# Optimization experiments

Measured on AMD Instinct MI355X. Metric: run time of the kernel, lower is better.

## Reference

```python
import jax, jax.numpy as jnp
import numpy as np

H, F = 4, 32          # num_of_heads, num_out_features
HF = H * F            # 128
F_IN = 128
EDGE_DIM = 64
HIDDEN = 256
B = 64
MLE = 1500
N = B * MLE           # 96000
E = 600000
LN_EPS = 1e-5


def setup_inputs() -> dict:
    key = jax.random.key(0)
    ks = jax.random.split(key, 20)

    def glorot(k, shape):
        fan_in, fan_out = shape[-2], shape[-1]
        lim = np.sqrt(6.0 / (fan_in + fan_out))
        return jax.random.uniform(k, shape, jnp.float32, -lim, lim)

    inp = {
        "in_nodes_features": jax.random.normal(ks[0], (N, F_IN), jnp.float32),
        "edge_index": jax.random.randint(ks[1], (2, E), 0, N),
        "edges": jax.random.normal(ks[2], (E, EDGE_DIM), jnp.float32),
        "instructions": jax.random.normal(ks[3], (B, HIDDEN), jnp.float32),
        "batch_ids": jax.random.randint(ks[4], (E,), 0, B),
        "max_local_entity": MLE,
        # parameters (stored as [in, out]; torch Linear is x @ W.T)
        "W_proj": glorot(ks[5], (F_IN, HF)),
        "W_edge": glorot(ks[6], (EDGE_DIM, HF)),
        "W_src_ins": glorot(ks[7], (HIDDEN, HF)),
        "b_src_ins": jnp.zeros((HF,), jnp.float32),
        "W_trg_ins": glorot(ks[8], (HIDDEN, HF)),
        "b_trg_ins": jnp.zeros((HF,), jnp.float32),
        "W_edge_ins": glorot(ks[9], (HIDDEN, HF)),
        "b_edge_ins": jnp.zeros((HF,), jnp.float32),
        "a_src": glorot(ks[10], (1, H, F)),
        "a_trg": glorot(ks[11], (1, H, F)),
        "a_edge": glorot(ks[12], (1, H, F)),
        "bias": jnp.zeros((HF,), jnp.float32),
        "W_skip": glorot(ks[13], (F_IN, HF)),
        "ln_gamma": jnp.ones((2 * HF,), jnp.float32),
        "ln_beta": jnp.zeros((2 * HF,), jnp.float32),
    }
    return inp


def _segment_softmax(scores, seg_idx, num_nodes):
    # scores: [E, H]; softmax over edges sharing the same seg_idx node
    s = scores - jax.lax.stop_gradient(scores.max())  # global-max shift, as in original
    e = jnp.exp(s)
    denom = jax.ops.segment_sum(e, seg_idx, num_segments=num_nodes)  # [N, H]
    return (e / (denom[seg_idx] + 1e-16))[..., None]  # [E, H, 1]


def _branch(proj, lift_idx, agg_idx, scores_per_edge, x, W_skip, bias, num_nodes):
    att = _segment_softmax(scores_per_edge, agg_idx, num_nodes)          # [E,H,1]
    weighted = proj[lift_idx] * att                                      # [E,H,F]
    out = jax.ops.segment_sum(weighted, agg_idx, num_segments=num_nodes) # [N,H,F]
    out = out + (x @ W_skip).reshape(num_nodes, H, F)                    # skip (F != F_in path)
    out = out.reshape(num_nodes, HF) + bias                              # concat heads + bias
    return out


def reference(in_nodes_features, edge_index, edges, instructions, batch_ids,
              max_local_entity, W_proj, W_edge, W_src_ins, b_src_ins,
              W_trg_ins, b_trg_ins, W_edge_ins, b_edge_ins,
              a_src, a_trg, a_edge, bias, W_skip, ln_gamma, ln_beta):
    x = in_nodes_features                      # dropout disabled (eval / p=0)
    num_nodes = x.shape[0]
    b = instructions.shape[0]
    src_idx, trg_idx = edge_index[0], edge_index[1]

    proj = (x @ W_proj).reshape(num_nodes, H, F)           # [N,H,F]
    eproj = (edges @ W_edge).reshape(-1, H, F)             # [E,H,F]

    def bridge(Wi, bi):  # instruction -> per-node [N,H,F]
        br = instructions @ Wi + bi                        # [B,HF]
        br = jnp.broadcast_to(br[:, None, :], (b, max_local_entity, HF))
        return br.reshape(num_nodes, H, F)

    src_br = bridge(W_src_ins, b_src_ins)
    trg_br = bridge(W_trg_ins, b_trg_ins)
    edge_br = (instructions @ W_edge_ins + b_edge_ins)[batch_ids].reshape(-1, H, F)

    scores_source = (proj * a_src * src_br).sum(-1)        # [N,H]
    scores_target = (proj * a_trg * trg_br).sum(-1)        # [N,H]
    scores_edge = (eproj * a_edge * edge_br).sum(-1)       # [E,H]

    scores_per_edge = jax.nn.leaky_relu(
        scores_source[src_idx] + scores_target[trg_idx] + scores_edge,
        negative_slope=0.2)                                # [E,H]

    # direction == 'all': aggregate src->trg and trg->src
    trg_feats = _branch(proj, src_idx, trg_idx, scores_per_edge, x, W_skip, bias, num_nodes)
    src_feats = _branch(proj, trg_idx, src_idx, scores_per_edge, x, W_skip, bias, num_nodes)

    out = jnp.concatenate([src_feats, trg_feats], axis=1)  # [N, 2*HF]
    mu = out.mean(-1, keepdims=True)
    var = ((out - mu) ** 2).mean(-1, keepdims=True)
    return (out - mu) * jax.lax.rsqrt(var + LN_EPS) * ln_gamma + ln_beta
```

## Files before the change

kernel.cpp:

```cpp
#include <hip/hip_runtime.h>
#include <stdint.h>

typedef unsigned short ushortT;
typedef __attribute__((ext_vector_type(8))) short short8;
typedef __attribute__((ext_vector_type(4))) float float4_;

#define HH 4
#define FF 32
#define HFD 128
#define F_IN 128
#define EDGE_DIM 64
#define HIDDEN 256
#define BB 64
#define MLE 1500
#define NN 96000
#define EEc 600000
#define CAP 32

__device__ __forceinline__ float bf_lo(uint32_t u){ return __uint_as_float(u << 16); }
__device__ __forceinline__ float bf_hi(uint32_t u){ return __uint_as_float(u & 0xffff0000u); }
__device__ __forceinline__ uint32_t f2bf(float f){
    uint32_t u = __float_as_uint(f);
    return (u + 0x7fffu + ((u >> 16) & 1u)) >> 16;
}
__device__ __forceinline__ short8 cvt8(const float* p){
    float4_ x0 = *(const float4_*)p;
    float4_ x1 = *(const float4_*)(p + 4);
    short8 r;
    r[0]=(short)f2bf(x0[0]); r[1]=(short)f2bf(x0[1]); r[2]=(short)f2bf(x0[2]); r[3]=(short)f2bf(x0[3]);
    r[4]=(short)f2bf(x1[0]); r[5]=(short)f2bf(x1[1]); r[6]=(short)f2bf(x1[2]); r[7]=(short)f2bf(x1[3]);
    return r;
}

__global__ void k_bridge(const float* ins, const float* Wsrc, const float* bsrc,
                         const float* Wtrg, const float* btrg,
                         const float* Wedg, const float* bedg,
                         const float* a_src, const float* a_trg, const float* a_edge,
                         const float* W_edge,
                         float* csrc, float* ctrg, float* Mout)
{
    __shared__ float ins_s[HIDDEN];
    __shared__ float ce_s[HFD];
    int b = blockIdx.x, t = threadIdx.x;
    const float* ip = ins + b * HIDDEN;
    ins_s[t]       = ip[t];
    ins_s[t + 128] = ip[t + 128];
    __syncthreads();
    float as = 0.f, at = 0.f, ae = 0.f;
    #pragma unroll 8
    for (int k = 0; k < HIDDEN; k++){
        float iv = ins_s[k];
        as += iv * Wsrc[k*HFD + t];
        at += iv * Wtrg[k*HFD + t];
        ae += iv * Wedg[k*HFD + t];
    }
    csrc[b*HFD + t] = (as + bsrc[t]) * a_src[t];
    ctrg[b*HFD + t] = (at + btrg[t]) * a_trg[t];
    ce_s[t] = (ae + bedg[t]) * a_edge[t];
    __syncthreads();
    #pragma unroll
    for (int rep = 0; rep < 2; rep++){
        int idx = t + rep * 128;
        int d = idx >> 2, h = idx & 3;
        float acc = 0.f;
        #pragma unroll
        for (int f = 0; f < FF; f++)
            acc += W_edge[d*HFD + h*FF + f] * ce_s[h*FF + f];
        Mout[b*256 + h*64 + d] = acc;
    }
}

__global__ void k_transpose(const float* Wp, const float* Wsk, ushortT* WcatT)
{
    int idx = blockIdx.x * 256 + threadIdx.x;
    int c = idx >> 7;
    int d = idx & 127;
    float v = (c < 128) ? Wp[d*128 + c] : Wsk[d*128 + (c - 128)];
    WcatT[c*128 + d] = (ushortT)f2bf(v);
}

__global__ __launch_bounds__(256) void k_gemm(const float* x, const ushortT* WcatT,
                                              const float* csrc, const float* ctrg,
                                              ushortT* proj, ushortT* skip,
                                              float* s_src, float* s_trg)
{
    int t = threadIdx.x;
    int w = t >> 6, lane = t & 63;
    int q = lane >> 4, n16 = lane & 15;
    size_t node = (size_t)blockIdx.x * 64 + w * 16 + n16;

    float4_ acc[16];
    #pragma unroll
    for (int j = 0; j < 16; j++) acc[j] = (float4_){0.f, 0.f, 0.f, 0.f};

    #pragma unroll
    for (int kk = 0; kk < 4; kk++){
        short8 bfrag = cvt8(x + node * 128 + kk*32 + q*8);
        #pragma unroll
        for (int j = 0; j < 16; j++){
            short8 afrag = *(const short8*)(WcatT + (size_t)(j*16 + n16) * 128 + kk*32 + q*8);
            acc[j] = __builtin_amdgcn_mfma_f32_16x16x32_bf16(afrag, bfrag, acc[j], 0, 0, 0);
        }
    }

    #pragma unroll
    for (int j = 0; j < 16; j++){
        uint32_t p0 = f2bf(acc[j][0]) | (f2bf(acc[j][1]) << 16);
        uint32_t p1 = f2bf(acc[j][2]) | (f2bf(acc[j][3]) << 16);
        ushortT* base = (j < 8) ? (proj + node*128 + j*16 + q*4)
                                : (skip + node*128 + (j-8)*16 + q*4);
        uint2 pv; pv.x = p0; pv.y = p1;
        *(uint2*)base = pv;
    }

    int b = (int)(node / MLE);
    const float* cs = csrc + b * HFD;
    const float* ct = ctrg + b * HFD;
    float ps[4] = {0,0,0,0}, pt[4] = {0,0,0,0};
    #pragma unroll
    for (int j = 0; j < 8; j++){
        int h = j >> 1;
        #pragma unroll
        for (int r = 0; r < 4; r++){
            int c = j*16 + q*4 + r;
            ps[h] += acc[j][r] * cs[c];
            pt[h] += acc[j][r] * ct[c];
        }
    }
    #pragma unroll
    for (int m = 16; m < 64; m <<= 1){
        #pragma unroll
        for (int hh = 0; hh < 4; hh++){
            ps[hh] += __shfl_xor(ps[hh], m, 64);
            pt[hh] += __shfl_xor(pt[hh], m, 64);
        }
    }
    float vs = (q == 0) ? ps[0] : (q == 1) ? ps[1] : (q == 2) ? ps[2] : ps[3];
    float vt = (q == 0) ? pt[0] : (q == 1) ? pt[1] : (q == 2) ? pt[2] : pt[3];
    s_src[node*4 + q] = vs;
    s_trg[node*4 + q] = vt;
}

__global__ __launch_bounds__(256) void k_score(const int* eidx, const int* bids,
    const float* edges, const float* M, const float* s_src, const float* s_trg,
    uint4* recs, int* head_src, int* head_trg, int* next_src, int* next_trg)
{
    int t = threadIdx.x;
    int wave = t >> 6, l = t & 63;
    int g = l >> 4, s = l & 15;
    int eb = (blockIdx.x * 4 + wave) * 16;

    int i_sel = s >> 2;
    int h_sel = s & 3;
    int e   = eb + i_sel*4 + g;
    int src = eidx[e];
    int trg = eidx[EEc + e];
    float ssv = s_src[(size_t)src*4 + h_sel];
    float stv = s_trg[(size_t)trg*4 + h_sel];

    float4_ ev[4];
    int bidv[4];
    #pragma unroll
    for (int i = 0; i < 4; i++){
        int r = i*4 + g;
        ev[i]   = *(const float4_*)(edges + (size_t)(eb + r) * 64 + s*4);
        bidv[i] = bids[eb + r];
    }

    float p00=0.f,p01=0.f,p02=0.f,p03=0.f;
    float p10=0.f,p11=0.f,p12=0.f,p13=0.f;
    float p20=0.f,p21=0.f,p22=0.f,p23=0.f;
    float p30=0.f,p31=0.f,p32=0.f,p33=0.f;
    #pragma unroll
    for (int i = 0; i < 4; i++){
        const float* Mb = M + (size_t)bidv[i] * 256;
        float4_ m0 = *(const float4_*)(Mb +   0 + s*4);
        float4_ m1 = *(const float4_*)(Mb +  64 + s*4);
        float4_ m2 = *(const float4_*)(Mb + 128 + s*4);
        float4_ m3 = *(const float4_*)(Mb + 192 + s*4);
        float4_ e4 = ev[i];
        float d0 = e4[0]*m0[0] + e4[1]*m0[1] + e4[2]*m0[2] + e4[3]*m0[3];
        float d1 = e4[0]*m1[0] + e4[1]*m1[1] + e4[2]*m1[2] + e4[3]*m1[3];
        float d2 = e4[0]*m2[0] + e4[1]*m2[1] + e4[2]*m2[2] + e4[3]*m2[3];
        float d3 = e4[0]*m3[0] + e4[1]*m3[1] + e4[2]*m3[2] + e4[3]*m3[3];
        if (i == 0){ p00=d0; p01=d1; p02=d2; p03=d3; }
        if (i == 1){ p10=d0; p11=d1; p12=d2; p13=d3; }
        if (i == 2){ p20=d0; p21=d1; p22=d2; p23=d3; }
        if (i == 3){ p30=d0; p31=d1; p32=d2; p33=d3; }
    }

    #pragma unroll
    for (int mm = 1; mm < 16; mm <<= 1){
        p00 += __shfl_xor(p00, mm, 64); p01 += __shfl_xor(p01, mm, 64);
        p02 += __shfl_xor(p02, mm, 64); p03 += __shfl_xor(p03, mm, 64);
        p10 += __shfl_xor(p10, mm, 64); p11 += __shfl_xor(p11, mm, 64);
        p12 += __shfl_xor(p12, mm, 64); p13 += __shfl_xor(p13, mm, 64);
        p20 += __shfl_xor(p20, mm, 64); p21 += __shfl_xor(p21, mm, 64);
        p22 += __shfl_xor(p22, mm, 64); p23 += __shfl_xor(p23, mm, 64);
        p30 += __shfl_xor(p30, mm, 64); p31 += __shfl_xor(p31, mm, 64);
        p32 += __shfl_xor(p32, mm, 64); p33 += __shfl_xor(p33, mm, 64);
    }

    float q0 = h_sel==0 ? p00 : h_sel==1 ? p01 : h_sel==2 ? p02 : p03;
    float q1 = h_sel==0 ? p10 : h_sel==1 ? p11 : h_sel==2 ? p12 : p13;
    float q2 = h_sel==0 ? p20 : h_sel==1 ? p21 : h_sel==2 ? p22 : p23;
    float q3 = h_sel==0 ? p30 : h_sel==1 ? p31 : h_sel==2 ? p32 : p33;
    float se = i_sel==0 ? q0 : i_sel==1 ? q1 : i_sel==2 ? q2 : q3;

    float sc = ssv + stv + se;
    sc = sc > 0.f ? sc : 0.2f * sc;
    float exv = __expf(sc);

    uint32_t my   = f2bf(exv) << ((h_sel & 1) * 16);
    uint32_t pair = my | __shfl_xor(my, 1, 64);
    uint32_t both = __shfl_xor(pair, 2, 64);

    if (h_sel == 0){
        uint4 rec;
        rec.x = (uint32_t)src; rec.y = (uint32_t)trg;
        rec.z = pair; rec.w = both;
        recs[e] = rec;
        int old0 = atomicExch(&head_src[src], e);
        next_src[e] = old0;
        int old1 = atomicExch(&head_trg[trg], e);
        next_trg[e] = old1;
    }
}

__global__ __launch_bounds__(256) void k_walk(const int* head_src, const int* head_trg,
    const int* next_src, const int* next_trg, const uint4* recs,
    int* cnt_src, int* cnt_trg, uint32_t* nbrT, uint2* evT)
{
    int id = blockIdx.x * 256 + threadIdx.x;
    int dir = (id >= NN) ? 1 : 0;
    int n = id - dir * NN;
    int e = dir ? head_trg[n] : head_src[n];
    const int* nx = dir ? next_trg : next_src;
    uint32_t* nT = nbrT + (size_t)dir * CAP * NN;
    uint2*    eT = evT  + (size_t)dir * CAP * NN;
    int c = 0;
    while (e >= 0 && c < CAP){
        uint4 r = recs[e];
        int en = nx[e];
        nT[(size_t)c*NN + n] = dir ? r.x : r.y;
        eT[(size_t)c*NN + n] = make_uint2(r.z, r.w);
        e = en;
        c++;
    }
    if (dir) cnt_trg[n] = c; else cnt_src[n] = c;
}

__global__ __launch_bounds__(256) void k_agg(const ushortT* proj, const ushortT* skip,
    const float* bias,
    const int* cnt_src, const int* cnt_trg,
    const uint32_t* nbrT, const uint2* evT,
    const float* gamma, const float* beta, float* out)
{
    __shared__ int   sh_nbr[2][4][CAP];
    __shared__ float sh_ev [2][4][CAP*4];

    int wave = threadIdx.x >> 6, lane = threadIdx.x & 63;
    int n = blockIdx.x * 4 + wave;
    int h = lane >> 4;

    int cnt0 = cnt_src[n]; if (cnt0 > CAP) cnt0 = CAP;
    int cnt1 = cnt_trg[n]; if (cnt1 > CAP) cnt1 = CAP;

    if (lane < cnt0){
        uint32_t nbr = nbrT[(size_t)lane*NN + n];
        uint2 e2     = evT [(size_t)lane*NN + n];
        sh_nbr[0][wave][lane] = (int)nbr;
        float4_ evv = { bf_lo(e2.x), bf_hi(e2.x), bf_lo(e2.y), bf_hi(e2.y) };
        *(float4_*)&sh_ev[0][wave][lane*4] = evv;
    }
    if (lane < cnt1){
        uint32_t nbr = nbrT[(size_t)(CAP + lane)*NN + n];
        uint2 e2     = evT [(size_t)(CAP + lane)*NN + n];
        sh_nbr[1][wave][lane] = (int)nbr;
        float4_ evv = { bf_lo(e2.x), bf_hi(e2.x), bf_lo(e2.y), bf_hi(e2.y) };
        *(float4_*)&sh_ev[1][wave][lane*4] = evv;
    }

    uint32_t sv = ((const uint32_t*)(skip + (size_t)n * 128))[lane];
    float b0 = bias[2*lane], b1 = bias[2*lane + 1];

    __syncthreads();

    float sk0 = bf_lo(sv) + b0;
    float sk1 = bf_hi(sv) + b1;

    float a0 = 0.f, a1 = 0.f, ad = 0.f;
    #pragma unroll 4
    for (int i = 0; i < cnt0; i++){
        int nbr  = sh_nbr[0][wave][i];
        float evw = sh_ev[0][wave][i*4 + h];
        uint32_t pv = ((const uint32_t*)(proj + (size_t)nbr * 128))[lane];
        a0 += evw * bf_lo(pv);
        a1 += evw * bf_hi(pv);
        ad += evw;
    }
    float inv = 1.f / (ad + 1e-16f);
    float f0 = a0 * inv + sk0;
    float f1 = a1 * inv + sk1;

    a0 = 0.f; a1 = 0.f; ad = 0.f;
    #pragma unroll 4
    for (int i = 0; i < cnt1; i++){
        int nbr  = sh_nbr[1][wave][i];
        float evw = sh_ev[1][wave][i*4 + h];
        uint32_t pv = ((const uint32_t*)(proj + (size_t)nbr * 128))[lane];
        a0 += evw * bf_lo(pv);
        a1 += evw * bf_hi(pv);
        ad += evw;
    }
    inv = 1.f / (ad + 1e-16f);
    float f2 = a0 * inv + sk0;
    float f3 = a1 * inv + sk1;

    float sum = f0 + f1 + f2 + f3;
    float sq  = f0*f0 + f1*f1 + f2*f2 + f3*f3;
    #pragma unroll
    for (int m = 1; m < 64; m <<= 1){
        sum += __shfl_xor(sum, m, 64);
        sq  += __shfl_xor(sq,  m, 64);
    }
    float mu  = sum * (1.f/256.f);
    float var = sq * (1.f/256.f) - mu*mu;
    var = var < 0.f ? 0.f : var;
    float rr = rsqrtf(var + 1e-5f);

    float o0 = (f0 - mu) * rr * gamma[2*lane]           + beta[2*lane];
    float o1 = (f1 - mu) * rr * gamma[2*lane + 1]       + beta[2*lane + 1];
    float o2 = (f2 - mu) * rr * gamma[128 + 2*lane]     + beta[128 + 2*lane];
    float o3 = (f3 - mu) * rr * gamma[128 + 2*lane + 1] + beta[128 + 2*lane + 1];

    float* orow = out + (size_t)n * 256;
    *(float2*)(orow + 2*lane)       = make_float2(o0, o1);
    *(float2*)(orow + 128 + 2*lane) = make_float2(o2, o3);
}

extern "C" void kernel_launch(void* const* d_in, const int* in_sizes, int n_in,
                              void* d_out, int out_size, void* d_ws, size_t ws_size,
                              hipStream_t stream)
{
    const float* x      = (const float*)d_in[0];
    const int*   eidx   = (const int*)d_in[1];
    const float* edges  = (const float*)d_in[2];
    const float* ins    = (const float*)d_in[3];
    const int*   bids   = (const int*)d_in[4];
    const float* Wproj  = (const float*)d_in[6];
    const float* Wedge  = (const float*)d_in[7];
    const float* Wsrc   = (const float*)d_in[8];
    const float* bsrc   = (const float*)d_in[9];
    const float* Wtrg   = (const float*)d_in[10];
    const float* btrg   = (const float*)d_in[11];
    const float* Wedgi  = (const float*)d_in[12];
    const float* bedgi  = (const float*)d_in[13];
    const float* a_src  = (const float*)d_in[14];
    const float* a_trg  = (const float*)d_in[15];
    const float* a_edge = (const float*)d_in[16];
    const float* bias   = (const float*)d_in[17];
    const float* Wskip  = (const float*)d_in[18];
    const float* gamma  = (const float*)d_in[19];
    const float* beta   = (const float*)d_in[20];

    char* ws = (char*)d_ws;
    size_t off = 0;
    ushortT* proj  = (ushortT*)(ws + off); off += (size_t)NN * 128 * 2;
    ushortT* skip  = (ushortT*)(ws + off); off += (size_t)NN * 128 * 2;
    ushortT* WcatT = (ushortT*)(ws + off); off += 256 * 128 * 2;
    float*   csrc  = (float*)(ws + off);   off += BB * HFD * 4;
    float*   ctrg  = (float*)(ws + off);   off += BB * HFD * 4;
    float*   M     = (float*)(ws + off);   off += BB * 256 * 4;
    float*   s_src = (float*)(ws + off);   off += (size_t)NN * 4 * 4;
    float*   s_trg = (float*)(ws + off);   off += (size_t)NN * 4 * 4;
    int*     cnt_src = (int*)(ws + off);   off += (size_t)NN * 4;
    int*     cnt_trg = (int*)(ws + off);   off += (size_t)NN * 4;
    int*     head_src = (int*)(ws + off);  off += (size_t)NN * 4;
    int*     head_trg = (int*)(ws + off);  off += (size_t)NN * 4;
    int*     next_src = (int*)(ws + off);  off += (size_t)EEc * 4;
    int*     next_trg = (int*)(ws + off);  off += (size_t)EEc * 4;
    uint4*   recs  = (uint4*)(ws + off);   off += (size_t)EEc * 16;
    uint32_t* nbrT = (uint32_t*)(ws + off); off += (size_t)2 * CAP * NN * 4;
    uint2*   evT   = (uint2*)(ws + off);   off += (size_t)2 * CAP * NN * 8;

    hipMemsetAsync(head_src, 0xFF, (size_t)NN * 4 * 2, stream);

    k_bridge<<<dim3(BB), dim3(128), 0, stream>>>(ins, Wsrc, bsrc, Wtrg, btrg, Wedgi, bedgi,
                                                 a_src, a_trg, a_edge, Wedge, csrc, ctrg, M);
    k_transpose<<<dim3(128), dim3(256), 0, stream>>>(Wproj, Wskip, WcatT);
    k_gemm<<<dim3(NN/64), dim3(256), 0, stream>>>(x, WcatT, csrc, ctrg, proj, skip, s_src, s_trg);
    k_score<<<dim3(EEc/64), dim3(256), 0, stream>>>(eidx, bids, edges, M, s_src, s_trg,
                                                    recs, head_src, head_trg, next_src, next_trg);
    k_walk<<<dim3(2*NN/256), dim3(256), 0, stream>>>(head_src, head_trg, next_src, next_trg,
                                                     recs, cnt_src, cnt_trg, nbrT, evT);
    k_agg<<<dim3(NN/4), dim3(256), 0, stream>>>(proj, skip, bias, cnt_src, cnt_trg,
                                                nbrT, evT, gamma, beta, (float*)d_out);
}
```

Before: 540.4 us.

## Move linked-list head atomics from score kernel into GEMM kernel

The atomic exchanges that build the per-node edge linked lists now run inside the GEMM kernel. Each of its 384000 threads handles up to two edges, and the atomic latency is meant to overlap with the MFMA work. The next-pointer stores are deferred to the end of the GEMM so the atomics stay in flight while it computes. The score kernel loses its atomics and issues its edge-feature and batch-id loads earlier. In exchange the GEMM kernel takes more registers and memory traffic, which could lower its occupancy.

```diff
diff --git a/kernel.cpp b/kernel.cpp
--- a/kernel.cpp
+++ b/kernel.cpp
@@ -16,6 +16,7 @@
 #define NN 96000
 #define EEc 600000
 #define CAP 32
+#define GEMM_THREADS (NN/64*256)
 
 __device__ __forceinline__ float bf_lo(uint32_t u){ return __uint_as_float(u << 16); }
 __device__ __forceinline__ float bf_hi(uint32_t u){ return __uint_as_float(u & 0xffff0000u); }
@@ -82,12 +83,29 @@
 __global__ __launch_bounds__(256) void k_gemm(const float* x, const ushortT* WcatT,
                                               const float* csrc, const float* ctrg,
                                               ushortT* proj, ushortT* skip,
-                                              float* s_src, float* s_trg)
+                                              float* s_src, float* s_trg,
+                                              const int* eidx,
+                                              int* head_src, int* head_trg,
+                                              int* next_src, int* next_trg)
 {
     int t = threadIdx.x;
     int w = t >> 6, lane = t & 63;
     int q = lane >> 4, n16 = lane & 15;
     size_t node = (size_t)blockIdx.x * 64 + w * 16 + n16;
+
+    int tid = blockIdx.x * 256 + t;
+    int eA = tid, eB = tid + GEMM_THREADS;
+    int sA = eidx[eA], tA = eidx[EEc + eA];
+    bool hasB = (eB < EEc);
+    int sB = 0, tB = 0;
+    if (hasB){ sB = eidx[eB]; tB = eidx[EEc + eB]; }
+    int oldSA = atomicExch(&head_src[sA], eA);
+    int oldTA = atomicExch(&head_trg[tA], eA);
+    int oldSB = 0, oldTB = 0;
+    if (hasB){
+        oldSB = atomicExch(&head_src[sB], eB);
+        oldTB = atomicExch(&head_trg[tB], eB);
+    }
 
     float4_ acc[16];
     #pragma unroll
@@ -139,16 +157,33 @@
     float vt = (q == 0) ? pt[0] : (q == 1) ? pt[1] : (q == 2) ? pt[2] : pt[3];
     s_src[node*4 + q] = vs;
     s_trg[node*4 + q] = vt;
+
+    next_src[eA] = oldSA;
+    next_trg[eA] = oldTA;
+    if (hasB){
+        next_src[eB] = oldSB;
+        next_trg[eB] = oldTB;
+    }
 }
 
 __global__ __launch_bounds__(256) void k_score(const int* eidx, const int* bids,
     const float* edges, const float* M, const float* s_src, const float* s_trg,
-    uint4* recs, int* head_src, int* head_trg, int* next_src, int* next_trg)
+    uint4* recs)
 {
     int t = threadIdx.x;
     int wave = t >> 6, l = t & 63;
     int g = l >> 4, s = l & 15;
     int eb = (blockIdx.x * 4 + wave) * 16;
+
+    float4_ ev[4];
+    #pragma unroll
+    for (int i = 0; i < 4; i++)
+        ev[i] = *(const float4_*)(edges + (size_t)(eb + i*4 + g) * 64 + s*4);
+
+    int bidv[4];
+    #pragma unroll
+    for (int i = 0; i < 4; i++)
+        bidv[i] = bids[eb + i*4 + g];
 
     int i_sel = s >> 2;
     int h_sel = s & 3;
@@ -157,15 +192,6 @@
     int trg = eidx[EEc + e];
     float ssv = s_src[(size_t)src*4 + h_sel];
     float stv = s_trg[(size_t)trg*4 + h_sel];
-
-    float4_ ev[4];
-    int bidv[4];
-    #pragma unroll
-    for (int i = 0; i < 4; i++){
-        int r = i*4 + g;
-        ev[i]   = *(const float4_*)(edges + (size_t)(eb + r) * 64 + s*4);
-        bidv[i] = bids[eb + r];
-    }
 
     float p00=0.f,p01=0.f,p02=0.f,p03=0.f;
     float p10=0.f,p11=0.f,p12=0.f,p13=0.f;
@@ -220,10 +246,6 @@
         rec.x = (uint32_t)src; rec.y = (uint32_t)trg;
         rec.z = pair; rec.w = both;
         recs[e] = rec;
-        int old0 = atomicExch(&head_src[src], e);
-        next_src[e] = old0;
-        int old1 = atomicExch(&head_trg[trg], e);
-        next_trg[e] = old1;
     }
 }
 
@@ -389,9 +411,9 @@
     k_bridge<<<dim3(BB), dim3(128), 0, stream>>>(ins, Wsrc, bsrc, Wtrg, btrg, Wedgi, bedgi,
                                                  a_src, a_trg, a_edge, Wedge, csrc, ctrg, M);
     k_transpose<<<dim3(128), dim3(256), 0, stream>>>(Wproj, Wskip, WcatT);
-    k_gemm<<<dim3(NN/64), dim3(256), 0, stream>>>(x, WcatT, csrc, ctrg, proj, skip, s_src, s_trg);
-    k_score<<<dim3(EEc/64), dim3(256), 0, stream>>>(eidx, bids, edges, M, s_src, s_trg,
-                                                    recs, head_src, head_trg, next_src, next_trg);
+    k_gemm<<<dim3(NN/64), dim3(256), 0, stream>>>(x, WcatT, csrc, ctrg, proj, skip, s_src, s_trg,
+                                                  eidx, head_src, head_trg, next_src, next_trg);
+    k_score<<<dim3(EEc/64), dim3(256), 0, stream>>>(eidx, bids, edges, M, s_src, s_trg, recs);
     k_walk<<<dim3(2*NN/256), dim3(256), 0, stream>>>(head_src, head_trg, next_src, next_trg,
                                                      recs, cnt_src, cnt_trg, nbrT, evT);
     k_agg<<<dim3(NN/4), dim3(256), 0, stream>>>(proj, skip, bias, cnt_src, cnt_trg,
```

Result: no change. 547.8 us (+1.4%).
